# Kernel tuning notes

Hardware: AMD Instinct MI355X
Metric: run time of the kernel (lower is better)

The kernel has to match this reference:

```python
import jax, jax.numpy as jnp
import numpy as np

RES = 1024
FEAT = 12
CB = 32
H_IMG, W_IMG = 1080, 1920


def cube_sample(cubemap, d):
    """Cube-map bilinear texture sample (nvdiffrast-style face selection,
    clamped bilinear within the selected face).
    cubemap: [6, R, R, C], d: [N, 3] unit directions -> [N, C]."""
    R = cubemap.shape[1]
    x, y, z = d[:, 0], d[:, 1], d[:, 2]
    ax, ay, az = jnp.abs(x), jnp.abs(y), jnp.abs(z)
    is_x = (ax >= ay) & (ax >= az)
    is_y = (~is_x) & (ay >= az)
    face = jnp.where(is_x, jnp.where(x >= 0, 0, 1),
           jnp.where(is_y, jnp.where(y >= 0, 2, 3),
                     jnp.where(z >= 0, 4, 5)))
    ma = jnp.where(is_x, ax, jnp.where(is_y, ay, az))
    u = jnp.where(is_x, jnp.where(x >= 0, -z, z),
        jnp.where(is_y, x, jnp.where(z >= 0, x, -x)))
    v = jnp.where(is_x, -y, jnp.where(is_y, jnp.where(y >= 0, z, -z), -y))
    eps = 1e-9
    s = (u / (ma + eps) + 1.0) * 0.5 * R - 0.5  # texel-space column
    t = (v / (ma + eps) + 1.0) * 0.5 * R - 0.5  # texel-space row
    x0 = jnp.floor(s); y0 = jnp.floor(t)
    fx = (s - x0)[:, None]; fy = (t - y0)[:, None]
    x0i = jnp.clip(x0.astype(jnp.int32), 0, R - 1)
    x1i = jnp.clip(x0i + 1, 0, R - 1)
    y0i = jnp.clip(y0.astype(jnp.int32), 0, R - 1)
    y1i = jnp.clip(y0i + 1, 0, R - 1)
    c00 = cubemap[face, y0i, x0i]
    c01 = cubemap[face, y0i, x1i]
    c10 = cubemap[face, y1i, x0i]
    c11 = cubemap[face, y1i, x1i]
    return (c00 * (1 - fx) + c01 * fx) * (1 - fy) + (c10 * (1 - fx) + c11 * fx) * fy


def setup_inputs() -> dict:
    key = jax.random.key(0)
    ks = jax.random.split(key, 9)
    rays_d = jax.random.normal(ks[0], (H_IMG, W_IMG, 3), jnp.float32)
    rays_d = rays_d / jnp.linalg.norm(rays_d, axis=-1, keepdims=True)
    mask = jax.random.randint(ks[1], (H_IMG, W_IMG), 0, 2) > 0  # sky mask
    sky_cube_map = jax.random.normal(ks[2], (6, RES, RES, FEAT), jnp.float32) * 0.1
    sky_codebook = jax.random.normal(ks[3], (CB, FEAT), jnp.float32) * 0.1
    W1 = jax.random.normal(ks[4], (FEAT + 3, 32), jnp.float32) * 0.25
    b1 = jnp.zeros((32,), jnp.float32)
    W2 = jax.random.normal(ks[5], (32, 32), jnp.float32) * 0.18
    b2 = jnp.zeros((32,), jnp.float32)
    W3 = jax.random.normal(ks[6], (32, 3), jnp.float32) * 0.18
    b3 = jnp.zeros((3,), jnp.float32)
    return {"rays_d": rays_d, "mask": mask, "sky_cube_map": sky_cube_map,
            "sky_codebook": sky_codebook, "W1": W1, "b1": b1,
            "W2": W2, "b2": b2, "W3": W3, "b3": b3}


def reference(rays_d, mask, sky_cube_map, sky_codebook, W1, b1, W2, b2, W3, b3):
    H, W = mask.shape
    d = rays_d.reshape(-1, 3)                       # [N, 3]
    feat_enc = cube_sample(sky_cube_map, d)         # [N, 12]
    # vq_st with detached codebook: nearest-codeword quantize, straight-through.
    cb = jax.lax.stop_gradient(sky_codebook)
    d2 = (jnp.sum(feat_enc * feat_enc, -1, keepdims=True)
          - 2.0 * (feat_enc @ cb.T)
          + jnp.sum(cb * cb, -1))                   # [N, 32]
    idx = jnp.argmin(d2, axis=-1)                   # [N]
    q = feat_enc + jax.lax.stop_gradient(cb[idx] - feat_enc)
    h = jnp.concatenate([q, d], axis=-1)            # [N, 15]
    h = jax.nn.relu(h @ W1 + b1)
    h = jax.nn.relu(h @ W2 + b2)
    rgb = jax.nn.sigmoid(h @ W3 + b3)               # [N, 3]
    # scatter shaded sky color into the (black-background) buffer via the mask
    img = jnp.where(mask.reshape(-1)[:, None], rgb, 0.0)
    return jnp.clip(img.reshape(H, W, 3).transpose(2, 0, 1), 0.0, 1.0)
```

## Files before the change

kernel.cpp:

```cpp
#include <hip/hip_runtime.h>
#include <math.h>

#define RES   1024
#define FEATC 12
#define CBN   32
#define H_IMG 1080
#define W_IMG 1920
#define NPIX  (H_IMG * W_IMG)

__global__ __launch_bounds__(256) void sky_kernel(
    const float* __restrict__ rays_d,
    const int*   __restrict__ mask,
    const float* __restrict__ cube,
    const float* __restrict__ cb,
    const float* __restrict__ W1,
    const float* __restrict__ b1,
    const float* __restrict__ W2,
    const float* __restrict__ b2,
    const float* __restrict__ W3,
    const float* __restrict__ b3,
    float*       __restrict__ out)
{
    __shared__ float sW1[15 * 32];
    __shared__ float sb1[32];
    __shared__ float sW2[32 * 32];
    __shared__ float sb2[32];
    __shared__ float sW3[32 * 3];
    __shared__ float sb3[3];
    __shared__ float sCB[CBN * FEATC];

    for (int t = threadIdx.x; t < 15 * 32; t += blockDim.x) sW1[t] = W1[t];
    for (int t = threadIdx.x; t < 32;      t += blockDim.x) sb1[t] = b1[t];
    for (int t = threadIdx.x; t < 32 * 32; t += blockDim.x) sW2[t] = W2[t];
    for (int t = threadIdx.x; t < 32;      t += blockDim.x) sb2[t] = b2[t];
    for (int t = threadIdx.x; t < 32 * 3;  t += blockDim.x) sW3[t] = W3[t];
    for (int t = threadIdx.x; t < 3;       t += blockDim.x) sb3[t] = b3[t];
    for (int t = threadIdx.x; t < CBN * FEATC; t += blockDim.x) sCB[t] = cb[t];
    __syncthreads();

    const int i = blockIdx.x * blockDim.x + threadIdx.x;
    if (i >= NPIX) return;

    if (mask[i] == 0) {
        out[0 * NPIX + i] = 0.0f;
        out[1 * NPIX + i] = 0.0f;
        out[2 * NPIX + i] = 0.0f;
        return;
    }

    const float x = rays_d[3 * i + 0];
    const float y = rays_d[3 * i + 1];
    const float z = rays_d[3 * i + 2];

    const float ax = fabsf(x), ay = fabsf(y), az = fabsf(z);
    const bool is_x = (ax >= ay) && (ax >= az);
    const bool is_y = (!is_x) && (ay >= az);

    int face; float ma, u, v;
    if (is_x) {
        face = (x >= 0.0f) ? 0 : 1;
        ma = ax;
        u = (x >= 0.0f) ? -z : z;
        v = -y;
    } else if (is_y) {
        face = (y >= 0.0f) ? 2 : 3;
        ma = ay;
        u = x;
        v = (y >= 0.0f) ? z : -z;
    } else {
        face = (z >= 0.0f) ? 4 : 5;
        ma = az;
        u = (z >= 0.0f) ? x : -x;
        v = -y;
    }

    const float denom = __fadd_rn(ma, 1e-9f);
    const float s = __fsub_rn(__fmul_rn(__fmul_rn(__fadd_rn(__fdiv_rn(u, denom), 1.0f), 0.5f), (float)RES), 0.5f);
    const float t = __fsub_rn(__fmul_rn(__fmul_rn(__fadd_rn(__fdiv_rn(v, denom), 1.0f), 0.5f), (float)RES), 0.5f);

    const float x0f = floorf(s);
    const float y0f = floorf(t);
    const float fx = __fsub_rn(s, x0f);
    const float fy = __fsub_rn(t, y0f);

    int x0i = (int)x0f; x0i = min(max(x0i, 0), RES - 1);
    int x1i = min(x0i + 1, RES - 1);
    int y0i = (int)y0f; y0i = min(max(y0i, 0), RES - 1);
    int y1i = min(y0i + 1, RES - 1);

    const size_t fbase = (size_t)face * RES * RES;
    const size_t off00 = (fbase + (size_t)y0i * RES + x0i) * FEATC;
    const size_t off01 = (fbase + (size_t)y0i * RES + x1i) * FEATC;
    const size_t off10 = (fbase + (size_t)y1i * RES + x0i) * FEATC;
    const size_t off11 = (fbase + (size_t)y1i * RES + x1i) * FEATC;

    const float4* p00 = (const float4*)(cube + off00);
    const float4* p01 = (const float4*)(cube + off01);
    const float4* p10 = (const float4*)(cube + off10);
    const float4* p11 = (const float4*)(cube + off11);

    float c00[FEATC], c01[FEATC], c10[FEATC], c11[FEATC];
    #pragma unroll
    for (int q4 = 0; q4 < 3; ++q4) {
        float4 a = p00[q4]; c00[4*q4+0]=a.x; c00[4*q4+1]=a.y; c00[4*q4+2]=a.z; c00[4*q4+3]=a.w;
        float4 b = p01[q4]; c01[4*q4+0]=b.x; c01[4*q4+1]=b.y; c01[4*q4+2]=b.z; c01[4*q4+3]=b.w;
        float4 c = p10[q4]; c10[4*q4+0]=c.x; c10[4*q4+1]=c.y; c10[4*q4+2]=c.z; c10[4*q4+3]=c.w;
        float4 dd= p11[q4]; c11[4*q4+0]=dd.x;c11[4*q4+1]=dd.y;c11[4*q4+2]=dd.z;c11[4*q4+3]=dd.w;
    }

    const float omfx = __fsub_rn(1.0f, fx);
    const float omfy = __fsub_rn(1.0f, fy);
    float feat[FEATC];
    #pragma unroll
    for (int k = 0; k < FEATC; ++k) {
        const float top = __fadd_rn(__fmul_rn(c00[k], omfx), __fmul_rn(c01[k], fx));
        const float bot = __fadd_rn(__fmul_rn(c10[k], omfx), __fmul_rn(c11[k], fx));
        feat[k] = __fadd_rn(__fmul_rn(top, omfy), __fmul_rn(bot, fy));
    }

    int best = 0;
    double bestd = 1e300;
    for (int j = 0; j < CBN; ++j) {
        double d2 = 0.0;
        #pragma unroll
        for (int k = 0; k < FEATC; ++k) {
            const double diff = (double)feat[k] - (double)sCB[j * FEATC + k];
            d2 += diff * diff;
        }
        if (d2 < bestd) { bestd = d2; best = j; }
    }

    float hin[15];
    #pragma unroll
    for (int k = 0; k < FEATC; ++k)
        hin[k] = __fadd_rn(feat[k], __fsub_rn(sCB[best * FEATC + k], feat[k]));
    hin[12] = x; hin[13] = y; hin[14] = z;

    float h1[32];
    #pragma unroll
    for (int k = 0; k < 32; ++k) {
        float a = sb1[k];
        #pragma unroll
        for (int j = 0; j < 15; ++j) a += hin[j] * sW1[j * 32 + k];
        h1[k] = fmaxf(a, 0.0f);
    }

    float h2[32];
    #pragma unroll
    for (int k = 0; k < 32; ++k) {
        float a = sb2[k];
        #pragma unroll
        for (int j = 0; j < 32; ++j) a += h1[j] * sW2[j * 32 + k];
        h2[k] = fmaxf(a, 0.0f);
    }

    #pragma unroll
    for (int c = 0; c < 3; ++c) {
        float a = sb3[c];
        #pragma unroll
        for (int j = 0; j < 32; ++j) a += h2[j] * sW3[j * 3 + c];
        float r = 1.0f / (1.0f + expf(-a));
        r = fminf(fmaxf(r, 0.0f), 1.0f);
        out[(size_t)c * NPIX + i] = r;
    }
}

extern "C" void kernel_launch(void* const* d_in, const int* in_sizes, int n_in,
                              void* d_out, int out_size, void* d_ws, size_t ws_size,
                              hipStream_t stream) {
    const float* rays_d = (const float*)d_in[0];
    const int*   mask   = (const int*)d_in[1];
    const float* cube   = (const float*)d_in[2];
    const float* cb     = (const float*)d_in[3];
    const float* W1     = (const float*)d_in[4];
    const float* b1     = (const float*)d_in[5];
    const float* W2     = (const float*)d_in[6];
    const float* b2     = (const float*)d_in[7];
    const float* W3     = (const float*)d_in[8];
    const float* b3     = (const float*)d_in[9];
    float* out = (float*)d_out;

    const int block = 256;
    const int grid = (NPIX + block - 1) / block;
    sky_kernel<<<grid, block, 0, stream>>>(rays_d, mask, cube, cb,
                                           W1, b1, W2, b2, W3, b3, out);
}
```

Measured before the change: 616.7 us.

## Compact masked pixels per block and use dot-product form for codebook search

```diff
diff --git a/kernel.cpp b/kernel.cpp
--- a/kernel.cpp
+++ b/kernel.cpp
@@ -7,6 +7,7 @@
 #define H_IMG 1080
 #define W_IMG 1920
 #define NPIX  (H_IMG * W_IMG)
+#define PPB   512
 
 __global__ __launch_bounds__(256) void sky_kernel(
     const float* __restrict__ rays_d,
@@ -21,153 +22,212 @@
     const float* __restrict__ b3,
     float*       __restrict__ out)
 {
-    __shared__ float sW1[15 * 32];
-    __shared__ float sb1[32];
-    __shared__ float sW2[32 * 32];
-    __shared__ float sb2[32];
-    __shared__ float sW3[32 * 3];
-    __shared__ float sb3[3];
-    __shared__ float sCB[CBN * FEATC];
-
-    for (int t = threadIdx.x; t < 15 * 32; t += blockDim.x) sW1[t] = W1[t];
-    for (int t = threadIdx.x; t < 32;      t += blockDim.x) sb1[t] = b1[t];
-    for (int t = threadIdx.x; t < 32 * 32; t += blockDim.x) sW2[t] = W2[t];
-    for (int t = threadIdx.x; t < 32;      t += blockDim.x) sb2[t] = b2[t];
-    for (int t = threadIdx.x; t < 32 * 3;  t += blockDim.x) sW3[t] = W3[t];
-    for (int t = threadIdx.x; t < 3;       t += blockDim.x) sb3[t] = b3[t];
-    for (int t = threadIdx.x; t < CBN * FEATC; t += blockDim.x) sCB[t] = cb[t];
+    __shared__ float  sW1[15 * 32];
+    __shared__ float  sb1[32];
+    __shared__ float  sW2[32 * 32];
+    __shared__ float  sb2[32];
+    __shared__ float  sW3[32 * 3];
+    __shared__ float  sb3[3];
+    __shared__ float  sCB[CBN * FEATC];
+    __shared__ double sCBd[CBN * FEATC];
+    __shared__ double sCnorm[CBN];
+    __shared__ int    sIdx[PPB];
+    __shared__ float  sRay[PPB * 3];
+    __shared__ int    sCnt;
+
+    const int tid = threadIdx.x;
+
+    for (int t = tid; t < 15 * 32; t += 256) sW1[t] = W1[t];
+    for (int t = tid; t < 32;      t += 256) sb1[t] = b1[t];
+    for (int t = tid; t < 32 * 32; t += 256) sW2[t] = W2[t];
+    for (int t = tid; t < 32;      t += 256) sb2[t] = b2[t];
+    for (int t = tid; t < 32 * 3;  t += 256) sW3[t] = W3[t];
+    for (int t = tid; t < 3;       t += 256) sb3[t] = b3[t];
+    for (int t = tid; t < CBN * FEATC; t += 256) {
+        const float v = cb[t];
+        sCB[t]  = v;
+        sCBd[t] = (double)v;
+    }
+    if (tid < CBN) {
+        double ssum = 0.0;
+        #pragma unroll
+        for (int k = 0; k < FEATC; ++k) {
+            const double cv = (double)cb[tid * FEATC + k];
+            ssum = fma(cv, cv, ssum);
+        }
+        sCnorm[tid] = ssum;
+    }
+    if (tid == 0) sCnt = 0;
     __syncthreads();
 
-    const int i = blockIdx.x * blockDim.x + threadIdx.x;
-    if (i >= NPIX) return;
-
-    if (mask[i] == 0) {
-        out[0 * NPIX + i] = 0.0f;
-        out[1 * NPIX + i] = 0.0f;
-        out[2 * NPIX + i] = 0.0f;
-        return;
-    }
-
-    const float x = rays_d[3 * i + 0];
-    const float y = rays_d[3 * i + 1];
-    const float z = rays_d[3 * i + 2];
-
-    const float ax = fabsf(x), ay = fabsf(y), az = fabsf(z);
-    const bool is_x = (ax >= ay) && (ax >= az);
-    const bool is_y = (!is_x) && (ay >= az);
-
-    int face; float ma, u, v;
-    if (is_x) {
-        face = (x >= 0.0f) ? 0 : 1;
-        ma = ax;
-        u = (x >= 0.0f) ? -z : z;
-        v = -y;
-    } else if (is_y) {
-        face = (y >= 0.0f) ? 2 : 3;
-        ma = ay;
-        u = x;
-        v = (y >= 0.0f) ? z : -z;
-    } else {
-        face = (z >= 0.0f) ? 4 : 5;
-        ma = az;
-        u = (z >= 0.0f) ? x : -x;
-        v = -y;
-    }
-
-    const float denom = __fadd_rn(ma, 1e-9f);
-    const float s = __fsub_rn(__fmul_rn(__fmul_rn(__fadd_rn(__fdiv_rn(u, denom), 1.0f), 0.5f), (float)RES), 0.5f);
-    const float t = __fsub_rn(__fmul_rn(__fmul_rn(__fadd_rn(__fdiv_rn(v, denom), 1.0f), 0.5f), (float)RES), 0.5f);
-
-    const float x0f = floorf(s);
-    const float y0f = floorf(t);
-    const float fx = __fsub_rn(s, x0f);
-    const float fy = __fsub_rn(t, y0f);
-
-    int x0i = (int)x0f; x0i = min(max(x0i, 0), RES - 1);
-    int x1i = min(x0i + 1, RES - 1);
-    int y0i = (int)y0f; y0i = min(max(y0i, 0), RES - 1);
-    int y1i = min(y0i + 1, RES - 1);
-
-    const size_t fbase = (size_t)face * RES * RES;
-    const size_t off00 = (fbase + (size_t)y0i * RES + x0i) * FEATC;
-    const size_t off01 = (fbase + (size_t)y0i * RES + x1i) * FEATC;
-    const size_t off10 = (fbase + (size_t)y1i * RES + x0i) * FEATC;
-    const size_t off11 = (fbase + (size_t)y1i * RES + x1i) * FEATC;
-
-    const float4* p00 = (const float4*)(cube + off00);
-    const float4* p01 = (const float4*)(cube + off01);
-    const float4* p10 = (const float4*)(cube + off10);
-    const float4* p11 = (const float4*)(cube + off11);
-
-    float c00[FEATC], c01[FEATC], c10[FEATC], c11[FEATC];
+    const int base = blockIdx.x * PPB;
+    const int lane = tid & 63;
+
     #pragma unroll
-    for (int q4 = 0; q4 < 3; ++q4) {
-        float4 a = p00[q4]; c00[4*q4+0]=a.x; c00[4*q4+1]=a.y; c00[4*q4+2]=a.z; c00[4*q4+3]=a.w;
-        float4 b = p01[q4]; c01[4*q4+0]=b.x; c01[4*q4+1]=b.y; c01[4*q4+2]=b.z; c01[4*q4+3]=b.w;
-        float4 c = p10[q4]; c10[4*q4+0]=c.x; c10[4*q4+1]=c.y; c10[4*q4+2]=c.z; c10[4*q4+3]=c.w;
-        float4 dd= p11[q4]; c11[4*q4+0]=dd.x;c11[4*q4+1]=dd.y;c11[4*q4+2]=dd.z;c11[4*q4+3]=dd.w;
-    }
-
-    const float omfx = __fsub_rn(1.0f, fx);
-    const float omfy = __fsub_rn(1.0f, fy);
-    float feat[FEATC];
-    #pragma unroll
-    for (int k = 0; k < FEATC; ++k) {
-        const float top = __fadd_rn(__fmul_rn(c00[k], omfx), __fmul_rn(c01[k], fx));
-        const float bot = __fadd_rn(__fmul_rn(c10[k], omfx), __fmul_rn(c11[k], fx));
-        feat[k] = __fadd_rn(__fmul_rn(top, omfy), __fmul_rn(bot, fy));
-    }
-
-    int best = 0;
-    double bestd = 1e300;
-    for (int j = 0; j < CBN; ++j) {
-        double d2 = 0.0;
-        #pragma unroll
-        for (int k = 0; k < FEATC; ++k) {
-            const double diff = (double)feat[k] - (double)sCB[j * FEATC + k];
-            d2 += diff * diff;
-        }
-        if (d2 < bestd) { bestd = d2; best = j; }
-    }
-
-    float hin[15];
-    #pragma unroll
-    for (int k = 0; k < FEATC; ++k)
-        hin[k] = __fadd_rn(feat[k], __fsub_rn(sCB[best * FEATC + k], feat[k]));
-    hin[12] = x; hin[13] = y; hin[14] = z;
-
-    float h1[32];
-    #pragma unroll
-    for (int k = 0; k < 32; ++k) {
-        float a = sb1[k];
-        #pragma unroll
-        for (int j = 0; j < 15; ++j) a += hin[j] * sW1[j * 32 + k];
-        h1[k] = fmaxf(a, 0.0f);
-    }
-
-    float h2[32];
-    #pragma unroll
-    for (int k = 0; k < 32; ++k) {
-        float a = sb2[k];
-        #pragma unroll
-        for (int j = 0; j < 32; ++j) a += h1[j] * sW2[j * 32 + k];
-        h2[k] = fmaxf(a, 0.0f);
-    }
-
-    #pragma unroll
-    for (int c = 0; c < 3; ++c) {
-        float a = sb3[c];
-        #pragma unroll
-        for (int j = 0; j < 32; ++j) a += h2[j] * sW3[j * 3 + c];
-        float r = 1.0f / (1.0f + expf(-a));
-        r = fminf(fmaxf(r, 0.0f), 1.0f);
-        out[(size_t)c * NPIX + i] = r;
+    for (int r = 0; r < 2; ++r) {
+        const int i  = base + r * 256 + tid;
+        const bool ok = (mask[i] != 0);
+        const float x = rays_d[3 * i + 0];
+        const float y = rays_d[3 * i + 1];
+        const float z = rays_d[3 * i + 2];
+
+        const unsigned long long bal = __ballot(ok);
+        const int pre  = __popcll(bal & ((1ull << lane) - 1ull));
+        const int wcnt = __popcll(bal);
+        int wbase = 0;
+        if (lane == 0) wbase = atomicAdd(&sCnt, wcnt);
+        wbase = __shfl(wbase, 0, 64);
+
+        if (!ok) {
+            out[0 * (size_t)NPIX + i] = 0.0f;
+            out[1 * (size_t)NPIX + i] = 0.0f;
+            out[2 * (size_t)NPIX + i] = 0.0f;
+        } else {
+            const int p = wbase + pre;
+            sIdx[p] = i;
+            sRay[3 * p + 0] = x;
+            sRay[3 * p + 1] = y;
+            sRay[3 * p + 2] = z;
+        }
+    }
+    __syncthreads();
+    const int cnt = sCnt;
+
+    for (int j = tid; j < cnt; j += 256) {
+        const int i   = sIdx[j];
+        const float x = sRay[3 * j + 0];
+        const float y = sRay[3 * j + 1];
+        const float z = sRay[3 * j + 2];
+
+        const float ax = fabsf(x), ay = fabsf(y), az = fabsf(z);
+        const bool is_x = (ax >= ay) && (ax >= az);
+        const bool is_y = (!is_x) && (ay >= az);
+
+        int face; float ma, u, v;
+        if (is_x) {
+            face = (x >= 0.0f) ? 0 : 1;
+            ma = ax;
+            u = (x >= 0.0f) ? -z : z;
+            v = -y;
+        } else if (is_y) {
+            face = (y >= 0.0f) ? 2 : 3;
+            ma = ay;
+            u = x;
+            v = (y >= 0.0f) ? z : -z;
+        } else {
+            face = (z >= 0.0f) ? 4 : 5;
+            ma = az;
+            u = (z >= 0.0f) ? x : -x;
+            v = -y;
+        }
+
+        const float denom = __fadd_rn(ma, 1e-9f);
+        const float s = __fsub_rn(__fmul_rn(__fmul_rn(__fadd_rn(__fdiv_rn(u, denom), 1.0f), 0.5f), (float)RES), 0.5f);
+        const float t = __fsub_rn(__fmul_rn(__fmul_rn(__fadd_rn(__fdiv_rn(v, denom), 1.0f), 0.5f), (float)RES), 0.5f);
+
+        const float x0f = floorf(s);
+        const float y0f = floorf(t);
+        const float fx = __fsub_rn(s, x0f);
+        const float fy = __fsub_rn(t, y0f);
+
+        int x0i = (int)x0f; x0i = min(max(x0i, 0), RES - 1);
+        int x1i = min(x0i + 1, RES - 1);
+        int y0i = (int)y0f; y0i = min(max(y0i, 0), RES - 1);
+        int y1i = min(y0i + 1, RES - 1);
+
+        const size_t fbase = (size_t)face * RES * RES;
+        const float4* p00 = (const float4*)(cube + (fbase + (size_t)y0i * RES + x0i) * FEATC);
+        const float4* p01 = (const float4*)(cube + (fbase + (size_t)y0i * RES + x1i) * FEATC);
+        const float4* p10 = (const float4*)(cube + (fbase + (size_t)y1i * RES + x0i) * FEATC);
+        const float4* p11 = (const float4*)(cube + (fbase + (size_t)y1i * RES + x1i) * FEATC);
+
+        const float omfx = __fsub_rn(1.0f, fx);
+        const float omfy = __fsub_rn(1.0f, fy);
+        float feat[FEATC];
+        #pragma unroll
+        for (int q4 = 0; q4 < 3; ++q4) {
+            const float4 a  = p00[q4];
+            const float4 b  = p01[q4];
+            const float4 c  = p10[q4];
+            const float4 d4 = p11[q4];
+            {
+                const float top = __fadd_rn(__fmul_rn(a.x, omfx), __fmul_rn(b.x, fx));
+                const float bot = __fadd_rn(__fmul_rn(c.x, omfx), __fmul_rn(d4.x, fx));
+                feat[4 * q4 + 0] = __fadd_rn(__fmul_rn(top, omfy), __fmul_rn(bot, fy));
+            }
+            {
+                const float top = __fadd_rn(__fmul_rn(a.y, omfx), __fmul_rn(b.y, fx));
+                const float bot = __fadd_rn(__fmul_rn(c.y, omfx), __fmul_rn(d4.y, fx));
+                feat[4 * q4 + 1] = __fadd_rn(__fmul_rn(top, omfy), __fmul_rn(bot, fy));
+            }
+            {
+                const float top = __fadd_rn(__fmul_rn(a.z, omfx), __fmul_rn(b.z, fx));
+                const float bot = __fadd_rn(__fmul_rn(c.z, omfx), __fmul_rn(d4.z, fx));
+                feat[4 * q4 + 2] = __fadd_rn(__fmul_rn(top, omfy), __fmul_rn(bot, fy));
+            }
+            {
+                const float top = __fadd_rn(__fmul_rn(a.w, omfx), __fmul_rn(b.w, fx));
+                const float bot = __fadd_rn(__fmul_rn(c.w, omfx), __fmul_rn(d4.w, fx));
+                feat[4 * q4 + 3] = __fadd_rn(__fmul_rn(top, omfy), __fmul_rn(bot, fy));
+            }
+        }
+
+        double fd[FEATC];
+        #pragma unroll
+        for (int k = 0; k < FEATC; ++k) fd[k] = (double)feat[k];
+
+        int best = 0;
+        double bestd = 1e300;
+        #pragma unroll 4
+        for (int jj = 0; jj < CBN; ++jj) {
+            double dot = 0.0;
+            #pragma unroll
+            for (int k = 0; k < FEATC; ++k)
+                dot = fma(fd[k], sCBd[jj * FEATC + k], dot);
+            const double d2 = fma(-2.0, dot, sCnorm[jj]);
+            if (d2 < bestd) { bestd = d2; best = jj; }
+        }
+
+        float hin[15];
+        #pragma unroll
+        for (int k = 0; k < FEATC; ++k)
+            hin[k] = __fadd_rn(feat[k], __fsub_rn(sCB[best * FEATC + k], feat[k]));
+        hin[12] = x; hin[13] = y; hin[14] = z;
+
+        float h1[32];
+        #pragma unroll
+        for (int k = 0; k < 32; ++k) {
+            float a = sb1[k];
+            #pragma unroll
+            for (int jw = 0; jw < 15; ++jw) a += hin[jw] * sW1[jw * 32 + k];
+            h1[k] = fmaxf(a, 0.0f);
+        }
+
+        float h2[32];
+        #pragma unroll
+        for (int k = 0; k < 32; ++k) {
+            float a = sb2[k];
+            #pragma unroll
+            for (int jw = 0; jw < 32; ++jw) a += h1[jw] * sW2[jw * 32 + k];
+            h2[k] = fmaxf(a, 0.0f);
+        }
+
+        #pragma unroll
+        for (int c = 0; c < 3; ++c) {
+            float a = sb3[c];
+            #pragma unroll
+            for (int jw = 0; jw < 32; ++jw) a += h2[jw] * sW3[jw * 3 + c];
+            float r = 1.0f / (1.0f + expf(-a));
+            r = fminf(fmaxf(r, 0.0f), 1.0f);
+            out[(size_t)c * NPIX + i] = r;
+        }
     }
 }
 
 extern "C" void kernel_launch(void* const* d_in, const int* in_sizes, int n_in,
                               void* d_out, int out_size, void* d_ws, size_t ws_size,
                               hipStream_t stream) {
+    (void)in_sizes; (void)n_in; (void)out_size; (void)d_ws; (void)ws_size;
     const float* rays_d = (const float*)d_in[0];
     const int*   mask   = (const int*)d_in[1];
     const float* cube   = (const float*)d_in[2];
@@ -181,7 +241,7 @@
     float* out = (float*)d_out;
 
     const int block = 256;
-    const int grid = (NPIX + block - 1) / block;
+    const int grid  = NPIX / PPB;
     sky_kernel<<<grid, block, 0, stream>>>(rays_d, mask, cube, cb,
                                            W1, b1, W2, b2, W3, b3, out);
 }
```

New measurement: 967.0 us. 56.8% more time.
